# Kernel optimization log

Hardware: AMD Instinct MI355X
Metric: run time of the kernel (lower is better)

## Reference

```python
import jax, jax.numpy as jnp
import numpy as np

L, B, N_IN, N_OUT, BIDIR, K = 2048, 16, 256, 256, 2, 6


def setup_inputs() -> dict:
    key = jax.random.key(0)
    k1, k2 = jax.random.split(key, 2)
    x = jax.random.normal(k1, (L, B, N_IN), jnp.float32)
    val = (6.0 / (N_IN + N_OUT)) ** 0.5
    weight_in = jax.random.uniform(k2, (N_IN, BIDIR * N_OUT * K), jnp.float32, -val, val)
    bias_in = jnp.zeros((K * BIDIR * N_OUT,), jnp.float32)
    c1_init = jnp.zeros((B, BIDIR * N_OUT), jnp.float32)
    c2_init = jnp.zeros((B, BIDIR * N_OUT), jnp.float32)
    d_init = jnp.zeros((B, BIDIR * N_OUT), jnp.float32)
    return {"x": x, "weight_in": weight_in, "bias_in": bias_in,
            "c1_init": c1_init, "c2_init": c2_init, "d_init": d_init}


def _flip_dir1(a):
    # reverse time for the backward direction (dir index 1)
    return a.at[:, :, 1].set(jnp.flip(a[:, :, 1], axis=0))


def _sopa_forward(x, weight_in, bias_in, c1_init, c2_init, d_init):
    length, batch = x.shape[0], x.shape[1]
    # u_: [L, B, bidir, n_out, k]
    u = (x.reshape(-1, N_IN) @ weight_in).reshape(length, batch, BIDIR, N_OUT, K)
    bias = bias_in.reshape(K, BIDIR, N_OUT)  # [k, bidir, n_out]
    x1, x2, x3 = u[..., 0], u[..., 1], u[..., 2]
    f1 = jax.nn.sigmoid(u[..., 3] + bias[3])
    f2 = jax.nn.sigmoid(u[..., 4] + bias[4])
    # selfloop gate sigmoid(u[...,5]+bias[5]) is computed in the original but
    # unused by the recurrence, so it is omitted here (no effect on outputs).

    # flip time for direction 1 so one scan handles both directions
    x1f, x2f, x3f, f1f, f2f = (_flip_dir1(a) for a in (x1, x2, x3, f1, f2))

    c1_0 = c1_init.reshape(batch, BIDIR, N_OUT)
    c2_0 = c2_init.reshape(batch, BIDIR, N_OUT)
    d_0 = d_init.reshape(batch, BIDIR, N_OUT)

    def step(carry, inp):
        c1, c2, d = carry
        x1t, x2t, x3t, f1t, f2t = inp
        c1n = (c1 - x1t) * f1t + x1t
        tmp = x3t * d
        c2n = (c2 - tmp) * f2t + tmp
        return (c1n, c2n, x2t), (c1n, c2n)

    (c1_f, c2_f, d_f), (c1s, c2s) = jax.lax.scan(
        step, (c1_0, c2_0, d_0), (x1f, x2f, x3f, f1f, f2f))

    c1s = _flip_dir1(c1s)
    c2s = _flip_dir1(c2s)
    return (c1s, c2s,
            c1_f.reshape(batch, -1), c2_f.reshape(batch, -1), d_f.reshape(batch, -1))


def reference(x, weight_in, bias_in, c1_init, c2_init, d_init):
    return _sopa_forward(x, weight_in, bias_in, c1_init, c2_init, d_init)
```

## Files before the change

kernel.cpp:

```cpp
#include <hip/hip_runtime.h>
#include <cstdint>
#include <cstddef>

typedef unsigned short u16;
typedef unsigned int u32;
typedef __bf16 bf16x8 __attribute__((ext_vector_type(8)));
typedef float f32x4 __attribute__((ext_vector_type(4)));

#define SL 2048
#define NCH 8192
#define SEGS 64
#define SEGLEN 32

#define OFF_C2S 16777216
#define OFF_C1F 33554432
#define OFF_C2F 33562624
#define OFF_DF  33570816

__device__ __forceinline__ float bf2f(u16 u) {
  union { u32 i; float f; } v; v.i = ((u32)u) << 16; return v.f;
}
__device__ __forceinline__ u16 f2bf(float f) {
  union { float f; u32 i; } v; v.f = f;
  u32 x = v.i;
  return (u16)((x + 0x7fffu + ((x >> 16) & 1u)) >> 16);
}

__global__ __launch_bounds__(256) void repack_kernel(
    const float* __restrict__ W, u16* __restrict__ Wt) {
  int idx = blockIdx.x * 256 + threadIdx.x;
  int kk = idx & 255;
  int rest = idx >> 8;
  int ch2 = rest & 511;
  int p = rest >> 9;
  Wt[idx] = f2bf(W[(size_t)kk * 3072 + (ch2 >> 8) * 1536 + (ch2 & 255) * 6 + p]);
}

__global__ __launch_bounds__(256) void gemm_kernel(
    const float* __restrict__ x, const u16* __restrict__ Wt,
    const float* __restrict__ bias, u16* __restrict__ buf,
    u16* __restrict__ X2B, int t0c, int CHT) {
  __shared__ __align__(16) u16 As[2048 * 8];
  __shared__ __align__(16) u16 Bs[1024 * 8];
  const int tid = threadIdx.x;
  const int lane = tid & 63;
  const int wave = tid >> 6;
  const int wr = wave >> 1, wc = wave & 1;
  const int l15 = lane & 15, l4 = lane >> 4;
  const int rt = blockIdx.x;
  const int ch0 = blockIdx.y * 128;
  const int dir = ch0 >> 8;

#pragma unroll
  for (int i = 0; i < 8; ++i) {
    int chunk = tid + i * 256;
    int kb = chunk >> 6, m = chunk & 63;
    int tf = t0c + rt * 4 + (m >> 4);
    int ot = dir ? (SL - 1 - tf) : tf;
    int row = ot * 16 + (m & 15);
    const float* src = x + (size_t)row * 256 + kb * 8;
    f32x4 a = *(const f32x4*)src;
    f32x4 b = *(const f32x4*)(src + 4);
    union { bf16x8 v; u16 s[8]; } h;
#pragma unroll
    for (int j = 0; j < 4; ++j) { h.s[j] = f2bf(a[j]); h.s[4 + j] = f2bf(b[j]); }
    *(bf16x8*)(As + (size_t)chunk * 8) = h.v;
  }

  const size_t pstride = (size_t)CHT * NCH;
  for (int p = 0; p < 5; ++p) {
    f32x4 acc[2][4];
#pragma unroll
    for (int i = 0; i < 2; ++i)
#pragma unroll
      for (int j = 0; j < 4; ++j) acc[i][j] = (f32x4){0.f, 0.f, 0.f, 0.f};

    for (int kt = 0; kt < 4; ++kt) {
      bf16x8 rg[4];
#pragma unroll
      for (int i = 0; i < 4; ++i) {
        int chunk = tid + i * 256;
        int kbl = chunk >> 7, c = chunk & 127;
        rg[i] = *(const bf16x8*)(
            Wt + ((size_t)(p * 512 + ch0 + c) * 256 + kt * 64 + kbl * 8));
      }
      __syncthreads();
#pragma unroll
      for (int i = 0; i < 4; ++i) {
        int chunk = tid + i * 256;
        *(bf16x8*)(Bs + (size_t)chunk * 8) = rg[i];
      }
      __syncthreads();
#pragma unroll
      for (int h = 0; h < 2; ++h) {
        bf16x8 af[2], bfr[4];
#pragma unroll
        for (int i = 0; i < 2; ++i) {
          int kb = kt * 8 + h * 4 + l4;
          int m = wr * 32 + i * 16 + l15;
          af[i] = *(const bf16x8*)(As + (size_t)(kb * 64 + m) * 8);
        }
#pragma unroll
        for (int j = 0; j < 4; ++j) {
          int kbl = h * 4 + l4;
          int c = wc * 64 + j * 16 + l15;
          bfr[j] = *(const bf16x8*)(Bs + (size_t)(kbl * 128 + c) * 8);
        }
#pragma unroll
        for (int i = 0; i < 2; ++i)
#pragma unroll
          for (int j = 0; j < 4; ++j)
            acc[i][j] = __builtin_amdgcn_mfma_f32_16x16x32_bf16(
                af[i], bfr[j], acc[i][j], 0, 0, 0);
      }
    }

    u16* pl = buf + (size_t)p * pstride;
#pragma unroll
    for (int j = 0; j < 4; ++j) {
      int ch2 = ch0 + wc * 64 + j * 16 + l15;
      float bv = (p >= 3) ? bias[p * 512 + ch2] : 0.f;
#pragma unroll
      for (int i = 0; i < 2; ++i) {
#pragma unroll
        for (int r = 0; r < 4; ++r) {
          int row = wr * 32 + i * 16 + l4 * 4 + r;
          int tl = rt * 4 + (row >> 4);
          int b = row & 15;
          float v = acc[i][j][r];
          if (p >= 3) v = 1.f / (1.f + __expf(-(v + bv)));
          u16 hv = f2bf(v);
          int ch = b * 512 + ch2;
          pl[(size_t)tl * NCH + ch] = hv;
          if (p == 1) {
            int tf = t0c + tl;
            if ((tf & 31) == 31) X2B[(size_t)(tf >> 5) * NCH + ch] = hv;
          }
        }
      }
    }
  }
}

__global__ __launch_bounds__(256) void scanA_kernel(
    const u16* __restrict__ buf, const float* __restrict__ d_init,
    const u16* __restrict__ X2B,
    float* __restrict__ A1, float* __restrict__ B1,
    float* __restrict__ A2, float* __restrict__ B2, int c, int CHT) {
  int bid = blockIdx.x;
  int sl = bid >> 5, chg = bid & 31;
  int ch = chg * 256 + threadIdx.x;
  int s = c * (CHT / 32) + sl;
  size_t pstride = (size_t)CHT * NCH;
  const u16* p0 = buf;
  const u16* p1 = buf + pstride;
  const u16* p2 = buf + 2 * pstride;
  const u16* p3 = buf + 3 * pstride;
  const u16* p4 = buf + 4 * pstride;
  float x2prev = (s == 0) ? d_init[ch]
                          : bf2f(X2B[(size_t)(s - 1) * NCH + ch]);
  float a1 = 1.f, b1 = 0.f, a2 = 1.f, b2 = 0.f;
  size_t idx = (size_t)(sl * 32) * NCH + ch;
#pragma unroll 4
  for (int tt = 0; tt < SEGLEN; ++tt, idx += NCH) {
    float x1 = bf2f(p0[idx]), x2 = bf2f(p1[idx]), x3 = bf2f(p2[idx]);
    float f1 = bf2f(p3[idx]), f2 = bf2f(p4[idx]);
    a1 *= f1; b1 = f1 * b1 + (1.f - f1) * x1;
    float tmp = x3 * x2prev;
    a2 *= f2; b2 = f2 * b2 + (1.f - f2) * tmp;
    x2prev = x2;
  }
  int o = s * NCH + ch;
  A1[o] = a1; B1[o] = b1; A2[o] = a2; B2[o] = b2;
}

__global__ __launch_bounds__(256) void scanB_kernel(
    const float* __restrict__ A1, const float* __restrict__ B1,
    const float* __restrict__ A2, const float* __restrict__ B2,
    const float* __restrict__ c1_init, const float* __restrict__ c2_init,
    const u16* __restrict__ X2B,
    float* __restrict__ C1c, float* __restrict__ C2c, float* __restrict__ out) {
  int ch = blockIdx.x * 256 + threadIdx.x;
  float c1 = c1_init[ch], c2 = c2_init[ch];
#pragma unroll 8
  for (int s = 0; s < SEGS; ++s) {
    int o = s * NCH + ch;
    C1c[o] = c1; C2c[o] = c2;
    c1 = A1[o] * c1 + B1[o];
    c2 = A2[o] * c2 + B2[o];
  }
  out[OFF_C1F + ch] = c1;
  out[OFF_C2F + ch] = c2;
  out[OFF_DF + ch] = bf2f(X2B[(size_t)63 * NCH + ch]);
}

__global__ __launch_bounds__(256) void scanC_kernel(
    const u16* __restrict__ buf, const float* __restrict__ d_init,
    const u16* __restrict__ X2B,
    const float* __restrict__ C1c, const float* __restrict__ C2c,
    float* __restrict__ out, int c, int CHT) {
  int bid = blockIdx.x;
  int sl = bid >> 5, chg = bid & 31;
  int ch = chg * 256 + threadIdx.x;
  int s = c * (CHT / 32) + sl;
  size_t pstride = (size_t)CHT * NCH;
  const u16* p0 = buf;
  const u16* p1 = buf + pstride;
  const u16* p2 = buf + 2 * pstride;
  const u16* p3 = buf + 3 * pstride;
  const u16* p4 = buf + 4 * pstride;
  float x2prev = (s == 0) ? d_init[ch]
                          : bf2f(X2B[(size_t)(s - 1) * NCH + ch]);
  float c1 = C1c[s * NCH + ch];
  float c2 = C2c[s * NCH + ch];
  int dir = (ch >> 8) & 1;
  size_t idx = (size_t)(sl * 32) * NCH + ch;
#pragma unroll 4
  for (int tt = 0; tt < SEGLEN; ++tt, idx += NCH) {
    float x1 = bf2f(p0[idx]), x2 = bf2f(p1[idx]), x3 = bf2f(p2[idx]);
    float f1 = bf2f(p3[idx]), f2 = bf2f(p4[idx]);
    c1 = f1 * c1 + (1.f - f1) * x1;
    float tmp = x3 * x2prev;
    c2 = f2 * c2 + (1.f - f2) * tmp;
    x2prev = x2;
    int tfl = s * 32 + tt;
    int t_out = dir ? (SL - 1 - tfl) : tfl;
    size_t oidx = (size_t)t_out * NCH + ch;
    out[oidx] = c1;
    out[OFF_C2S + oidx] = c2;
  }
}

extern "C" void kernel_launch(void* const* d_in, const int* in_sizes, int n_in,
                              void* d_out, int out_size, void* d_ws, size_t ws_size,
                              hipStream_t stream) {
  const float* x    = (const float*)d_in[0];
  const float* W    = (const float*)d_in[1];
  const float* bias = (const float*)d_in[2];
  const float* c1i  = (const float*)d_in[3];
  const float* c2i  = (const float*)d_in[4];
  const float* di   = (const float*)d_in[5];
  float* out = (float*)d_out;

  uint8_t* w8 = (uint8_t*)d_ws;
  u16* Wt  = (u16*)w8;
  u16* X2B = (u16*)(w8 + 1310720ull);
  float* A1  = (float*)(w8 + 2359296ull);
  float* B1  = A1 + SEGS * NCH;
  float* A2  = B1 + SEGS * NCH;
  float* B2  = A2 + SEGS * NCH;
  float* C1c = B2 + SEGS * NCH;
  float* C2c = C1c + SEGS * NCH;
  const size_t FIXED = 2359296ull + 6ull * 2097152ull;
  u16* buf = (u16*)(w8 + FIXED);

  int NCHUNK = 64;
  size_t avail = (ws_size > FIXED) ? (ws_size - FIXED) : 0;
  for (int nc = 1; nc <= 64; nc <<= 1) {
    size_t need = (size_t)5 * (SL / nc) * NCH * 2;
    if (need <= avail) { NCHUNK = nc; break; }
  }
  const int CHT = SL / NCHUNK;

  hipLaunchKernelGGL(repack_kernel, dim3(2560), dim3(256), 0, stream, W, Wt);
  for (int c = 0; c < NCHUNK; ++c) {
    hipLaunchKernelGGL(gemm_kernel, dim3(CHT / 4, 4), dim3(256), 0, stream,
                       x, Wt, bias, buf, X2B, c * CHT, CHT);
    hipLaunchKernelGGL(scanA_kernel, dim3(CHT), dim3(256), 0, stream,
                       buf, di, X2B, A1, B1, A2, B2, c, CHT);
  }
  hipLaunchKernelGGL(scanB_kernel, dim3(32), dim3(256), 0, stream,
                     A1, B1, A2, B2, c1i, c2i, X2B, C1c, C2c, out);
  for (int c = 0; c < NCHUNK; ++c) {
    if (NCHUNK > 1)
      hipLaunchKernelGGL(gemm_kernel, dim3(CHT / 4, 4), dim3(256), 0, stream,
                         x, Wt, bias, buf, X2B, c * CHT, CHT);
    hipLaunchKernelGGL(scanC_kernel, dim3(CHT), dim3(256), 0, stream,
                       buf, di, X2B, C1c, C2c, out, c, CHT);
  }
}
```

Measured before the change: 373.8 us.

## Vectorize scans to 8 channels per thread, load GEMM B fragments directly

The scan kernels now handle 8 consecutive channels per thread with 16-byte bf16 loads and float4 stores, which cuts the block count and the number of memory instructions. The GEMM drops the LDS staging of weights and its two barriers per k-tile, loading B fragments straight from global memory. Float to bf16 conversion now uses the packed v_cvt_pk_bf16_f32 instruction, and an added barrier fixes a missing sync after the A tile is written to shared memory. In exchange, scan parallelism drops to 128 channel-threads per segment group, which lowers occupancy, and the direct global B loads depend on cache hits.

```diff
diff --git a/kernel.cpp b/kernel.cpp
--- a/kernel.cpp
+++ b/kernel.cpp
@@ -24,6 +24,11 @@
   union { float f; u32 i; } v; v.f = f;
   u32 x = v.i;
   return (u16)((x + 0x7fffu + ((x >> 16) & 1u)) >> 16);
+}
+__device__ __forceinline__ u32 cvtpk(float lo, float hi) {
+  u32 r;
+  asm("v_cvt_pk_bf16_f32 %0, %1, %2" : "=v"(r) : "v"(lo), "v"(hi));
+  return r;
 }
 
 __global__ __launch_bounds__(256) void repack_kernel(
@@ -41,7 +46,6 @@
     const float* __restrict__ bias, u16* __restrict__ buf,
     u16* __restrict__ X2B, int t0c, int CHT) {
   __shared__ __align__(16) u16 As[2048 * 8];
-  __shared__ __align__(16) u16 Bs[1024 * 8];
   const int tid = threadIdx.x;
   const int lane = tid & 63;
   const int wave = tid >> 6;
@@ -61,11 +65,14 @@
     const float* src = x + (size_t)row * 256 + kb * 8;
     f32x4 a = *(const f32x4*)src;
     f32x4 b = *(const f32x4*)(src + 4);
-    union { bf16x8 v; u16 s[8]; } h;
-#pragma unroll
-    for (int j = 0; j < 4; ++j) { h.s[j] = f2bf(a[j]); h.s[4 + j] = f2bf(b[j]); }
+    union { bf16x8 v; u32 u[4]; } h;
+    h.u[0] = cvtpk(a[0], a[1]);
+    h.u[1] = cvtpk(a[2], a[3]);
+    h.u[2] = cvtpk(b[0], b[1]);
+    h.u[3] = cvtpk(b[2], b[3]);
     *(bf16x8*)(As + (size_t)chunk * 8) = h.v;
   }
+  __syncthreads();
 
   const size_t pstride = (size_t)CHT * NCH;
   for (int p = 0; p < 5; ++p) {
@@ -75,37 +82,22 @@
 #pragma unroll
       for (int j = 0; j < 4; ++j) acc[i][j] = (f32x4){0.f, 0.f, 0.f, 0.f};
 
+    const u16* Wp = Wt + (size_t)(p * 512 + ch0 + wc * 64 + l15) * 256;
+
+#pragma unroll
     for (int kt = 0; kt < 4; ++kt) {
-      bf16x8 rg[4];
-#pragma unroll
-      for (int i = 0; i < 4; ++i) {
-        int chunk = tid + i * 256;
-        int kbl = chunk >> 7, c = chunk & 127;
-        rg[i] = *(const bf16x8*)(
-            Wt + ((size_t)(p * 512 + ch0 + c) * 256 + kt * 64 + kbl * 8));
-      }
-      __syncthreads();
-#pragma unroll
-      for (int i = 0; i < 4; ++i) {
-        int chunk = tid + i * 256;
-        *(bf16x8*)(Bs + (size_t)chunk * 8) = rg[i];
-      }
-      __syncthreads();
 #pragma unroll
       for (int h = 0; h < 2; ++h) {
-        bf16x8 af[2], bfr[4];
-#pragma unroll
-        for (int i = 0; i < 2; ++i) {
-          int kb = kt * 8 + h * 4 + l4;
-          int m = wr * 32 + i * 16 + l15;
-          af[i] = *(const bf16x8*)(As + (size_t)(kb * 64 + m) * 8);
-        }
-#pragma unroll
-        for (int j = 0; j < 4; ++j) {
-          int kbl = h * 4 + l4;
-          int c = wc * 64 + j * 16 + l15;
-          bfr[j] = *(const bf16x8*)(Bs + (size_t)(kbl * 128 + c) * 8);
-        }
+        const int kb = kt * 8 + h * 4 + l4;
+        bf16x8 bfr[4];
+#pragma unroll
+        for (int j = 0; j < 4; ++j)
+          bfr[j] = *(const bf16x8*)(Wp + (size_t)j * 16 * 256 + kb * 8);
+        bf16x8 af[2];
+#pragma unroll
+        for (int i = 0; i < 2; ++i)
+          af[i] = *(const bf16x8*)(
+              As + (size_t)(kb * 64 + wr * 32 + i * 16 + l15) * 8);
 #pragma unroll
         for (int i = 0; i < 2; ++i)
 #pragma unroll
@@ -122,19 +114,26 @@
       float bv = (p >= 3) ? bias[p * 512 + ch2] : 0.f;
 #pragma unroll
       for (int i = 0; i < 2; ++i) {
-#pragma unroll
-        for (int r = 0; r < 4; ++r) {
-          int row = wr * 32 + i * 16 + l4 * 4 + r;
-          int tl = rt * 4 + (row >> 4);
-          int b = row & 15;
-          float v = acc[i][j][r];
-          if (p >= 3) v = 1.f / (1.f + __expf(-(v + bv)));
-          u16 hv = f2bf(v);
+        int tl = rt * 4 + wr * 2 + i;
+        int tf = t0c + tl;
+        bool rec = (p == 1) && ((tf & 31) == 31);
+#pragma unroll
+        for (int r = 0; r < 4; r += 2) {
+          float va = acc[i][j][r], vb = acc[i][j][r + 1];
+          if (p >= 3) {
+            va = 1.f / (1.f + __expf(-(va + bv)));
+            vb = 1.f / (1.f + __expf(-(vb + bv)));
+          }
+          u32 pk = cvtpk(va, vb);
+          int b = l4 * 4 + r;
           int ch = b * 512 + ch2;
-          pl[(size_t)tl * NCH + ch] = hv;
-          if (p == 1) {
-            int tf = t0c + tl;
-            if ((tf & 31) == 31) X2B[(size_t)(tf >> 5) * NCH + ch] = hv;
+          size_t o = (size_t)tl * NCH + ch;
+          pl[o] = (u16)pk;
+          pl[o + 512] = (u16)(pk >> 16);
+          if (rec) {
+            size_t xo = (size_t)(tf >> 5) * NCH + ch;
+            X2B[xo] = (u16)pk;
+            X2B[xo + 512] = (u16)(pk >> 16);
           }
         }
       }
@@ -148,30 +147,57 @@
     float* __restrict__ A1, float* __restrict__ B1,
     float* __restrict__ A2, float* __restrict__ B2, int c, int CHT) {
   int bid = blockIdx.x;
-  int sl = bid >> 5, chg = bid & 31;
-  int ch = chg * 256 + threadIdx.x;
+  int sl = bid >> 2, chb = bid & 3;
+  int ch = chb * 2048 + threadIdx.x * 8;
   int s = c * (CHT / 32) + sl;
   size_t pstride = (size_t)CHT * NCH;
-  const u16* p0 = buf;
-  const u16* p1 = buf + pstride;
-  const u16* p2 = buf + 2 * pstride;
-  const u16* p3 = buf + 3 * pstride;
-  const u16* p4 = buf + 4 * pstride;
-  float x2prev = (s == 0) ? d_init[ch]
-                          : bf2f(X2B[(size_t)(s - 1) * NCH + ch]);
-  float a1 = 1.f, b1 = 0.f, a2 = 1.f, b2 = 0.f;
-  size_t idx = (size_t)(sl * 32) * NCH + ch;
+  const u16* p0 = buf + (size_t)(sl * 32) * NCH + ch;
+
+  float x2p[8];
+  if (s == 0) {
+    f32x4 d0 = *(const f32x4*)(d_init + ch);
+    f32x4 d1 = *(const f32x4*)(d_init + ch + 4);
+#pragma unroll
+    for (int r = 0; r < 4; ++r) { x2p[r] = d0[r]; x2p[4 + r] = d1[r]; }
+  } else {
+    union { bf16x8 v; u16 s[8]; } xv;
+    xv.v = *(const bf16x8*)(X2B + (size_t)(s - 1) * NCH + ch);
+#pragma unroll
+    for (int r = 0; r < 8; ++r) x2p[r] = bf2f(xv.s[r]);
+  }
+
+  float a1[8], b1[8], a2[8], b2[8];
+#pragma unroll
+  for (int r = 0; r < 8; ++r) { a1[r] = 1.f; b1[r] = 0.f; a2[r] = 1.f; b2[r] = 0.f; }
+
 #pragma unroll 4
-  for (int tt = 0; tt < SEGLEN; ++tt, idx += NCH) {
-    float x1 = bf2f(p0[idx]), x2 = bf2f(p1[idx]), x3 = bf2f(p2[idx]);
-    float f1 = bf2f(p3[idx]), f2 = bf2f(p4[idx]);
-    a1 *= f1; b1 = f1 * b1 + (1.f - f1) * x1;
-    float tmp = x3 * x2prev;
-    a2 *= f2; b2 = f2 * b2 + (1.f - f2) * tmp;
-    x2prev = x2;
-  }
-  int o = s * NCH + ch;
-  A1[o] = a1; B1[o] = b1; A2[o] = a2; B2[o] = b2;
+  for (int tt = 0; tt < SEGLEN; ++tt) {
+    size_t off = (size_t)tt * NCH;
+    union U { bf16x8 v; u16 s[8]; } v0, v1, v2, v3, v4;
+    v0.v = *(const bf16x8*)(p0 + off);
+    v1.v = *(const bf16x8*)(p0 + pstride + off);
+    v2.v = *(const bf16x8*)(p0 + 2 * pstride + off);
+    v3.v = *(const bf16x8*)(p0 + 3 * pstride + off);
+    v4.v = *(const bf16x8*)(p0 + 4 * pstride + off);
+#pragma unroll
+    for (int r = 0; r < 8; ++r) {
+      float x1 = bf2f(v0.s[r]), x2 = bf2f(v1.s[r]), x3 = bf2f(v2.s[r]);
+      float f1 = bf2f(v3.s[r]), f2 = bf2f(v4.s[r]);
+      a1[r] *= f1; b1[r] = f1 * b1[r] + (1.f - f1) * x1;
+      float tmp = x3 * x2p[r];
+      a2[r] *= f2; b2[r] = f2 * b2[r] + (1.f - f2) * tmp;
+      x2p[r] = x2;
+    }
+  }
+  size_t o = (size_t)s * NCH + ch;
+  *(f32x4*)(A1 + o) = (f32x4){a1[0], a1[1], a1[2], a1[3]};
+  *(f32x4*)(A1 + o + 4) = (f32x4){a1[4], a1[5], a1[6], a1[7]};
+  *(f32x4*)(B1 + o) = (f32x4){b1[0], b1[1], b1[2], b1[3]};
+  *(f32x4*)(B1 + o + 4) = (f32x4){b1[4], b1[5], b1[6], b1[7]};
+  *(f32x4*)(A2 + o) = (f32x4){a2[0], a2[1], a2[2], a2[3]};
+  *(f32x4*)(A2 + o + 4) = (f32x4){a2[4], a2[5], a2[6], a2[7]};
+  *(f32x4*)(B2 + o) = (f32x4){b2[0], b2[1], b2[2], b2[3]};
+  *(f32x4*)(B2 + o + 4) = (f32x4){b2[4], b2[5], b2[6], b2[7]};
 }
 
 __global__ __launch_bounds__(256) void scanB_kernel(
@@ -200,34 +226,66 @@
     const float* __restrict__ C1c, const float* __restrict__ C2c,
     float* __restrict__ out, int c, int CHT) {
   int bid = blockIdx.x;
-  int sl = bid >> 5, chg = bid & 31;
-  int ch = chg * 256 + threadIdx.x;
+  int sl = bid >> 2, chb = bid & 3;
+  int ch = chb * 2048 + threadIdx.x * 8;
   int s = c * (CHT / 32) + sl;
   size_t pstride = (size_t)CHT * NCH;
-  const u16* p0 = buf;
-  const u16* p1 = buf + pstride;
-  const u16* p2 = buf + 2 * pstride;
-  const u16* p3 = buf + 3 * pstride;
-  const u16* p4 = buf + 4 * pstride;
-  float x2prev = (s == 0) ? d_init[ch]
-                          : bf2f(X2B[(size_t)(s - 1) * NCH + ch]);
-  float c1 = C1c[s * NCH + ch];
-  float c2 = C2c[s * NCH + ch];
+  const u16* p0 = buf + (size_t)(sl * 32) * NCH + ch;
   int dir = (ch >> 8) & 1;
-  size_t idx = (size_t)(sl * 32) * NCH + ch;
-#pragma unroll 4
-  for (int tt = 0; tt < SEGLEN; ++tt, idx += NCH) {
-    float x1 = bf2f(p0[idx]), x2 = bf2f(p1[idx]), x3 = bf2f(p2[idx]);
-    float f1 = bf2f(p3[idx]), f2 = bf2f(p4[idx]);
-    c1 = f1 * c1 + (1.f - f1) * x1;
-    float tmp = x3 * x2prev;
-    c2 = f2 * c2 + (1.f - f2) * tmp;
-    x2prev = x2;
+
+  float x2p[8];
+  if (s == 0) {
+    f32x4 d0 = *(const f32x4*)(d_init + ch);
+    f32x4 d1 = *(const f32x4*)(d_init + ch + 4);
+#pragma unroll
+    for (int r = 0; r < 4; ++r) { x2p[r] = d0[r]; x2p[4 + r] = d1[r]; }
+  } else {
+    union { bf16x8 v; u16 s[8]; } xv;
+    xv.v = *(const bf16x8*)(X2B + (size_t)(s - 1) * NCH + ch);
+#pragma unroll
+    for (int r = 0; r < 8; ++r) x2p[r] = bf2f(xv.s[r]);
+  }
+
+  float c1[8], c2[8];
+  {
+    size_t o = (size_t)s * NCH + ch;
+    f32x4 u0 = *(const f32x4*)(C1c + o);
+    f32x4 u1 = *(const f32x4*)(C1c + o + 4);
+    f32x4 w0 = *(const f32x4*)(C2c + o);
+    f32x4 w1 = *(const f32x4*)(C2c + o + 4);
+#pragma unroll
+    for (int r = 0; r < 4; ++r) {
+      c1[r] = u0[r]; c1[4 + r] = u1[r];
+      c2[r] = w0[r]; c2[4 + r] = w1[r];
+    }
+  }
+
+#pragma unroll 2
+  for (int tt = 0; tt < SEGLEN; ++tt) {
+    size_t off = (size_t)tt * NCH;
+    union U { bf16x8 v; u16 s[8]; } v0, v1, v2, v3, v4;
+    v0.v = *(const bf16x8*)(p0 + off);
+    v1.v = *(const bf16x8*)(p0 + pstride + off);
+    v2.v = *(const bf16x8*)(p0 + 2 * pstride + off);
+    v3.v = *(const bf16x8*)(p0 + 3 * pstride + off);
+    v4.v = *(const bf16x8*)(p0 + 4 * pstride + off);
+#pragma unroll
+    for (int r = 0; r < 8; ++r) {
+      float x1 = bf2f(v0.s[r]), x2 = bf2f(v1.s[r]), x3 = bf2f(v2.s[r]);
+      float f1 = bf2f(v3.s[r]), f2 = bf2f(v4.s[r]);
+      c1[r] = f1 * c1[r] + (1.f - f1) * x1;
+      float tmp = x3 * x2p[r];
+      c2[r] = f2 * c2[r] + (1.f - f2) * tmp;
+      x2p[r] = x2;
+    }
     int tfl = s * 32 + tt;
     int t_out = dir ? (SL - 1 - tfl) : tfl;
-    size_t oidx = (size_t)t_out * NCH + ch;
-    out[oidx] = c1;
-    out[OFF_C2S + oidx] = c2;
+    float* o1 = out + (size_t)t_out * NCH + ch;
+    *(f32x4*)o1       = (f32x4){c1[0], c1[1], c1[2], c1[3]};
+    *(f32x4*)(o1 + 4) = (f32x4){c1[4], c1[5], c1[6], c1[7]};
+    float* o2 = o1 + OFF_C2S;
+    *(f32x4*)o2       = (f32x4){c2[0], c2[1], c2[2], c2[3]};
+    *(f32x4*)(o2 + 4) = (f32x4){c2[4], c2[5], c2[6], c2[7]};
   }
 }
 
@@ -266,7 +324,7 @@
   for (int c = 0; c < NCHUNK; ++c) {
     hipLaunchKernelGGL(gemm_kernel, dim3(CHT / 4, 4), dim3(256), 0, stream,
                        x, Wt, bias, buf, X2B, c * CHT, CHT);
-    hipLaunchKernelGGL(scanA_kernel, dim3(CHT), dim3(256), 0, stream,
+    hipLaunchKernelGGL(scanA_kernel, dim3((CHT / 32) * 4), dim3(256), 0, stream,
                        buf, di, X2B, A1, B1, A2, B2, c, CHT);
   }
   hipLaunchKernelGGL(scanB_kernel, dim3(32), dim3(256), 0, stream,
@@ -275,7 +333,7 @@
     if (NCHUNK > 1)
       hipLaunchKernelGGL(gemm_kernel, dim3(CHT / 4, 4), dim3(256), 0, stream,
                          x, Wt, bias, buf, X2B, c * CHT, CHT);
-    hipLaunchKernelGGL(scanC_kernel, dim3(CHT), dim3(256), 0, stream,
+    hipLaunchKernelGGL(scanC_kernel, dim3((CHT / 32) * 4), dim3(256), 0, stream,
                        buf, di, X2B, C1c, C2c, out, c, CHT);
   }
 }
```

Measured after the change: 443.0 us. 1.19x slower.

## Fuse projection GEMM into segment scans, recompute GEMM instead of buffering activations

Applied to the files above, without the earlier changes.

Replaces the chunked GEMM-then-scan pipeline with two fused kernels that compute the projection with MFMA in registers and immediately run the segment scan, recomputing the GEMM in the final pass instead of storing bf16 activations. x is pre-converted to a bf16 layout and weights are repacked into MFMA fragment order so B fragments load directly from global memory without LDS. The d-carry dependence across segments is folded into a G2 coefficient so segment summaries no longer need the previous segment's x2, and outputs use nontemporal stores. This removes the large intermediate buffer traffic and many kernel launches, at the cost of doing the GEMM twice and reading fragments uncached through global memory.

```diff
diff --git a/kernel.cpp b/kernel.cpp
--- a/kernel.cpp
+++ b/kernel.cpp
@@ -10,224 +10,272 @@
 #define SL 2048
 #define NCH 8192
 #define SEGS 64
-#define SEGLEN 32
 
 #define OFF_C2S 16777216
 #define OFF_C1F 33554432
 #define OFF_C2F 33562624
 #define OFF_DF  33570816
 
-__device__ __forceinline__ float bf2f(u16 u) {
-  union { u32 i; float f; } v; v.i = ((u32)u) << 16; return v.f;
-}
 __device__ __forceinline__ u16 f2bf(float f) {
   union { float f; u32 i; } v; v.f = f;
   u32 x = v.i;
   return (u16)((x + 0x7fffu + ((x >> 16) & 1u)) >> 16);
 }
+__device__ __forceinline__ u32 cvtpk(float lo, float hi) {
+  u32 r;
+  asm("v_cvt_pk_bf16_f32 %0, %1, %2" : "=v"(r) : "v"(lo), "v"(hi));
+  return r;
+}
+__device__ __forceinline__ float sigmoidf(float v) {
+  return 1.f / (1.f + __expf(-v));
+}
+
+__global__ __launch_bounds__(256) void xconv_kernel(
+    const float* __restrict__ x, u16* __restrict__ xb) {
+  int t8 = blockIdx.x * 256 + threadIdx.x;
+  int kb = t8 & 31;
+  int b  = (t8 >> 5) & 15;
+  int ot = t8 >> 9;
+  const float* src = x + (((size_t)(ot * 16 + b)) << 8) + kb * 8;
+  f32x4 a = *(const f32x4*)src;
+  f32x4 c = *(const f32x4*)(src + 4);
+  union { bf16x8 v; u32 u[4]; } h;
+  h.u[0] = cvtpk(a[0], a[1]);
+  h.u[1] = cvtpk(a[2], a[3]);
+  h.u[2] = cvtpk(c[0], c[1]);
+  h.u[3] = cvtpk(c[2], c[3]);
+  *(bf16x8*)(xb + ((size_t)ot << 12) + kb * 128 + b * 8) = h.v;
+}
 
 __global__ __launch_bounds__(256) void repack_kernel(
     const float* __restrict__ W, u16* __restrict__ Wt) {
   int idx = blockIdx.x * 256 + threadIdx.x;
-  int kk = idx & 255;
-  int rest = idx >> 8;
-  int ch2 = rest & 511;
-  int p = rest >> 9;
+  int kk8 = idx & 7;
+  int lane = (idx >> 3) & 63;
+  int h  = (idx >> 9) & 1;
+  int kt = (idx >> 10) & 3;
+  int cg = (idx >> 12) & 31;
+  int p  = idx >> 17;
+  int ch2 = cg * 16 + (lane & 15);
+  int kk  = (kt * 8 + h * 4 + (lane >> 4)) * 8 + kk8;
   Wt[idx] = f2bf(W[(size_t)kk * 3072 + (ch2 >> 8) * 1536 + (ch2 & 255) * 6 + p]);
 }
 
-__global__ __launch_bounds__(256) void gemm_kernel(
-    const float* __restrict__ x, const u16* __restrict__ Wt,
-    const float* __restrict__ bias, u16* __restrict__ buf,
-    u16* __restrict__ X2B, int t0c, int CHT) {
-  __shared__ __align__(16) u16 As[2048 * 8];
-  __shared__ __align__(16) u16 Bs[1024 * 8];
+__global__ __launch_bounds__(256, 2) void fusedA_kernel(
+    const u16* __restrict__ xb, const u16* __restrict__ Wt,
+    const float* __restrict__ bias,
+    float* __restrict__ A1, float* __restrict__ B1,
+    float* __restrict__ A2, float* __restrict__ B2k,
+    float* __restrict__ G2, float* __restrict__ X2B) {
   const int tid = threadIdx.x;
   const int lane = tid & 63;
-  const int wave = tid >> 6;
-  const int wr = wave >> 1, wc = wave & 1;
+  const int wc = tid >> 6;
   const int l15 = lane & 15, l4 = lane >> 4;
-  const int rt = blockIdx.x;
-  const int ch0 = blockIdx.y * 128;
-  const int dir = ch0 >> 8;
-
-#pragma unroll
-  for (int i = 0; i < 8; ++i) {
-    int chunk = tid + i * 256;
-    int kb = chunk >> 6, m = chunk & 63;
-    int tf = t0c + rt * 4 + (m >> 4);
-    int ot = dir ? (SL - 1 - tf) : tf;
-    int row = ot * 16 + (m & 15);
-    const float* src = x + (size_t)row * 256 + kb * 8;
-    f32x4 a = *(const f32x4*)src;
-    f32x4 b = *(const f32x4*)(src + 4);
-    union { bf16x8 v; u16 s[8]; } h;
-#pragma unroll
-    for (int j = 0; j < 4; ++j) { h.s[j] = f2bf(a[j]); h.s[4 + j] = f2bf(b[j]); }
-    *(bf16x8*)(As + (size_t)chunk * 8) = h.v;
-  }
-
-  const size_t pstride = (size_t)CHT * NCH;
-  for (int p = 0; p < 5; ++p) {
-    f32x4 acc[2][4];
-#pragma unroll
-    for (int i = 0; i < 2; ++i)
-#pragma unroll
-      for (int j = 0; j < 4; ++j) acc[i][j] = (f32x4){0.f, 0.f, 0.f, 0.f};
-
+  const int s = blockIdx.x;
+  const int bc = blockIdx.y;
+  const int dir = bc >> 2;
+  const int ch2 = bc * 64 + wc * 16 + l15;
+  const int fb0 = (bc * 4 + wc) * 8;
+
+  const float bv3 = bias[1536 + ch2];
+  const float bv4 = bias[2048 + ch2];
+
+  float a1[4], b1[4], a2[4], b2[4], g2[4], x2p[4];
+#pragma unroll
+  for (int r = 0; r < 4; ++r) {
+    a1[r] = 1.f; b1[r] = 0.f; a2[r] = 1.f; b2[r] = 0.f;
+    g2[r] = 0.f; x2p[r] = 0.f;
+  }
+
+  for (int rt = 0; rt < 8; ++rt) {
+    const u16* ab0; const u16* ab1; const u16* ab2; const u16* ab3;
+    {
+      int tf = s * 32 + rt * 4;
+      int o0 = dir ? (SL - 1 - tf) : tf;
+      int o1 = dir ? (o0 - 1) : (o0 + 1);
+      int o2 = dir ? (o0 - 2) : (o0 + 2);
+      int o3 = dir ? (o0 - 3) : (o0 + 3);
+      size_t lo = (size_t)(l4 * 128 + l15 * 8);
+      ab0 = xb + ((size_t)o0 << 12) + lo;
+      ab1 = xb + ((size_t)o1 << 12) + lo;
+      ab2 = xb + ((size_t)o2 << 12) + lo;
+      ab3 = xb + ((size_t)o3 << 12) + lo;
+    }
+
+    f32x4 acc[5][4];
+#pragma unroll
+    for (int p = 0; p < 5; ++p)
+#pragma unroll
+      for (int i = 0; i < 4; ++i) acc[p][i] = (f32x4){0.f, 0.f, 0.f, 0.f};
+
+#pragma unroll
     for (int kt = 0; kt < 4; ++kt) {
-      bf16x8 rg[4];
-#pragma unroll
-      for (int i = 0; i < 4; ++i) {
-        int chunk = tid + i * 256;
-        int kbl = chunk >> 7, c = chunk & 127;
-        rg[i] = *(const bf16x8*)(
-            Wt + ((size_t)(p * 512 + ch0 + c) * 256 + kt * 64 + kbl * 8));
-      }
-      __syncthreads();
-#pragma unroll
-      for (int i = 0; i < 4; ++i) {
-        int chunk = tid + i * 256;
-        *(bf16x8*)(Bs + (size_t)chunk * 8) = rg[i];
-      }
-      __syncthreads();
 #pragma unroll
       for (int h = 0; h < 2; ++h) {
-        bf16x8 af[2], bfr[4];
-#pragma unroll
-        for (int i = 0; i < 2; ++i) {
-          int kb = kt * 8 + h * 4 + l4;
-          int m = wr * 32 + i * 16 + l15;
-          af[i] = *(const bf16x8*)(As + (size_t)(kb * 64 + m) * 8);
-        }
-#pragma unroll
-        for (int j = 0; j < 4; ++j) {
-          int kbl = h * 4 + l4;
-          int c = wc * 64 + j * 16 + l15;
-          bfr[j] = *(const bf16x8*)(Bs + (size_t)(kbl * 128 + c) * 8);
-        }
-#pragma unroll
-        for (int i = 0; i < 2; ++i)
-#pragma unroll
-          for (int j = 0; j < 4; ++j)
-            acc[i][j] = __builtin_amdgcn_mfma_f32_16x16x32_bf16(
-                af[i], bfr[j], acc[i][j], 0, 0, 0);
-      }
-    }
-
-    u16* pl = buf + (size_t)p * pstride;
-#pragma unroll
-    for (int j = 0; j < 4; ++j) {
-      int ch2 = ch0 + wc * 64 + j * 16 + l15;
-      float bv = (p >= 3) ? bias[p * 512 + ch2] : 0.f;
-#pragma unroll
-      for (int i = 0; i < 2; ++i) {
-#pragma unroll
-        for (int r = 0; r < 4; ++r) {
-          int row = wr * 32 + i * 16 + l4 * 4 + r;
-          int tl = rt * 4 + (row >> 4);
-          int b = row & 15;
-          float v = acc[i][j][r];
-          if (p >= 3) v = 1.f / (1.f + __expf(-(v + bv)));
-          u16 hv = f2bf(v);
-          int ch = b * 512 + ch2;
-          pl[(size_t)tl * NCH + ch] = hv;
-          if (p == 1) {
-            int tf = t0c + tl;
-            if ((tf & 31) == 31) X2B[(size_t)(tf >> 5) * NCH + ch] = hv;
-          }
+        const int kb4 = (kt * 8 + h * 4) * 128;
+        bf16x8 af[4];
+        af[0] = *(const bf16x8*)(ab0 + kb4);
+        af[1] = *(const bf16x8*)(ab1 + kb4);
+        af[2] = *(const bf16x8*)(ab2 + kb4);
+        af[3] = *(const bf16x8*)(ab3 + kb4);
+        const int fb = fb0 + kt * 2 + h;
+#pragma unroll
+        for (int p = 0; p < 5; ++p) {
+          bf16x8 bfr = *(const bf16x8*)(
+              Wt + (size_t)(p * 256 + fb) * 512 + lane * 8);
+#pragma unroll
+          for (int i = 0; i < 4; ++i)
+            acc[p][i] = __builtin_amdgcn_mfma_f32_16x16x32_bf16(
+                af[i], bfr, acc[p][i], 0, 0, 0);
         }
       }
     }
-  }
-}
-
-__global__ __launch_bounds__(256) void scanA_kernel(
-    const u16* __restrict__ buf, const float* __restrict__ d_init,
-    const u16* __restrict__ X2B,
-    float* __restrict__ A1, float* __restrict__ B1,
-    float* __restrict__ A2, float* __restrict__ B2, int c, int CHT) {
-  int bid = blockIdx.x;
-  int sl = bid >> 5, chg = bid & 31;
-  int ch = chg * 256 + threadIdx.x;
-  int s = c * (CHT / 32) + sl;
-  size_t pstride = (size_t)CHT * NCH;
-  const u16* p0 = buf;
-  const u16* p1 = buf + pstride;
-  const u16* p2 = buf + 2 * pstride;
-  const u16* p3 = buf + 3 * pstride;
-  const u16* p4 = buf + 4 * pstride;
-  float x2prev = (s == 0) ? d_init[ch]
-                          : bf2f(X2B[(size_t)(s - 1) * NCH + ch]);
-  float a1 = 1.f, b1 = 0.f, a2 = 1.f, b2 = 0.f;
-  size_t idx = (size_t)(sl * 32) * NCH + ch;
-#pragma unroll 4
-  for (int tt = 0; tt < SEGLEN; ++tt, idx += NCH) {
-    float x1 = bf2f(p0[idx]), x2 = bf2f(p1[idx]), x3 = bf2f(p2[idx]);
-    float f1 = bf2f(p3[idx]), f2 = bf2f(p4[idx]);
-    a1 *= f1; b1 = f1 * b1 + (1.f - f1) * x1;
-    float tmp = x3 * x2prev;
-    a2 *= f2; b2 = f2 * b2 + (1.f - f2) * tmp;
-    x2prev = x2;
-  }
-  int o = s * NCH + ch;
-  A1[o] = a1; B1[o] = b1; A2[o] = a2; B2[o] = b2;
+
+    const bool first = (rt == 0);
+#pragma unroll
+    for (int i = 0; i < 4; ++i) {
+#pragma unroll
+      for (int r = 0; r < 4; ++r) {
+        float x1 = acc[0][i][r], x2v = acc[1][i][r], x3 = acc[2][i][r];
+        float f1 = sigmoidf(acc[3][i][r] + bv3);
+        float f2 = sigmoidf(acc[4][i][r] + bv4);
+        a1[r] *= f1;
+        b1[r] = f1 * b1[r] + (1.f - f1) * x1;
+        float tmp = x3 * x2p[r];
+        a2[r] *= f2;
+        b2[r] = f2 * b2[r] + (1.f - f2) * tmp;
+        g2[r] = (first && i == 0) ? (1.f - f2) * x3 : g2[r] * f2;
+        x2p[r] = x2v;
+      }
+    }
+  }
+
+  const int chb = (l4 * 4) * 512 + ch2;
+  const size_t o = (size_t)s * NCH + chb;
+#pragma unroll
+  for (int r = 0; r < 4; ++r) {
+    size_t oo = o + (size_t)r * 512;
+    A1[oo] = a1[r]; B1[oo] = b1[r]; A2[oo] = a2[r];
+    B2k[oo] = b2[r]; G2[oo] = g2[r]; X2B[oo] = x2p[r];
+  }
 }
 
 __global__ __launch_bounds__(256) void scanB_kernel(
     const float* __restrict__ A1, const float* __restrict__ B1,
-    const float* __restrict__ A2, const float* __restrict__ B2,
+    const float* __restrict__ A2, const float* __restrict__ B2k,
+    const float* __restrict__ G2, const float* __restrict__ X2B,
     const float* __restrict__ c1_init, const float* __restrict__ c2_init,
-    const u16* __restrict__ X2B,
-    float* __restrict__ C1c, float* __restrict__ C2c, float* __restrict__ out) {
+    const float* __restrict__ d_init,
+    float* __restrict__ C1c, float* __restrict__ C2c,
+    float* __restrict__ out) {
   int ch = blockIdx.x * 256 + threadIdx.x;
-  float c1 = c1_init[ch], c2 = c2_init[ch];
+  float c1 = c1_init[ch], c2 = c2_init[ch], d0 = d_init[ch];
 #pragma unroll 8
   for (int s = 0; s < SEGS; ++s) {
     int o = s * NCH + ch;
     C1c[o] = c1; C2c[o] = c2;
     c1 = A1[o] * c1 + B1[o];
-    c2 = A2[o] * c2 + B2[o];
+    c2 = A2[o] * c2 + (B2k[o] + G2[o] * d0);
+    d0 = X2B[o];
   }
   out[OFF_C1F + ch] = c1;
   out[OFF_C2F + ch] = c2;
-  out[OFF_DF + ch] = bf2f(X2B[(size_t)63 * NCH + ch]);
-}
-
-__global__ __launch_bounds__(256) void scanC_kernel(
-    const u16* __restrict__ buf, const float* __restrict__ d_init,
-    const u16* __restrict__ X2B,
+  out[OFF_DF + ch] = d0;
+}
+
+__global__ __launch_bounds__(256, 2) void fusedC_kernel(
+    const u16* __restrict__ xb, const u16* __restrict__ Wt,
+    const float* __restrict__ bias, const float* __restrict__ d_init,
+    const float* __restrict__ X2B,
     const float* __restrict__ C1c, const float* __restrict__ C2c,
-    float* __restrict__ out, int c, int CHT) {
-  int bid = blockIdx.x;
-  int sl = bid >> 5, chg = bid & 31;
-  int ch = chg * 256 + threadIdx.x;
-  int s = c * (CHT / 32) + sl;
-  size_t pstride = (size_t)CHT * NCH;
-  const u16* p0 = buf;
-  const u16* p1 = buf + pstride;
-  const u16* p2 = buf + 2 * pstride;
-  const u16* p3 = buf + 3 * pstride;
-  const u16* p4 = buf + 4 * pstride;
-  float x2prev = (s == 0) ? d_init[ch]
-                          : bf2f(X2B[(size_t)(s - 1) * NCH + ch]);
-  float c1 = C1c[s * NCH + ch];
-  float c2 = C2c[s * NCH + ch];
-  int dir = (ch >> 8) & 1;
-  size_t idx = (size_t)(sl * 32) * NCH + ch;
-#pragma unroll 4
-  for (int tt = 0; tt < SEGLEN; ++tt, idx += NCH) {
-    float x1 = bf2f(p0[idx]), x2 = bf2f(p1[idx]), x3 = bf2f(p2[idx]);
-    float f1 = bf2f(p3[idx]), f2 = bf2f(p4[idx]);
-    c1 = f1 * c1 + (1.f - f1) * x1;
-    float tmp = x3 * x2prev;
-    c2 = f2 * c2 + (1.f - f2) * tmp;
-    x2prev = x2;
-    int tfl = s * 32 + tt;
-    int t_out = dir ? (SL - 1 - tfl) : tfl;
-    size_t oidx = (size_t)t_out * NCH + ch;
-    out[oidx] = c1;
-    out[OFF_C2S + oidx] = c2;
+    float* __restrict__ out) {
+  const int tid = threadIdx.x;
+  const int lane = tid & 63;
+  const int wc = tid >> 6;
+  const int l15 = lane & 15, l4 = lane >> 4;
+  const int s = blockIdx.x;
+  const int bc = blockIdx.y;
+  const int dir = bc >> 2;
+  const int ch2 = bc * 64 + wc * 16 + l15;
+  const int fb0 = (bc * 4 + wc) * 8;
+
+  const float bv3 = bias[1536 + ch2];
+  const float bv4 = bias[2048 + ch2];
+
+  const int chb = (l4 * 4) * 512 + ch2;
+  float c1[4], c2[4], x2p[4];
+  {
+    size_t o = (size_t)s * NCH + chb;
+#pragma unroll
+    for (int r = 0; r < 4; ++r) {
+      c1[r] = C1c[o + r * 512];
+      c2[r] = C2c[o + r * 512];
+      x2p[r] = (s == 0) ? d_init[chb + r * 512] : X2B[o - NCH + r * 512];
+    }
+  }
+
+  for (int rt = 0; rt < 8; ++rt) {
+    const u16* ab0; const u16* ab1; const u16* ab2; const u16* ab3;
+    {
+      int tf = s * 32 + rt * 4;
+      int o0 = dir ? (SL - 1 - tf) : tf;
+      int o1 = dir ? (o0 - 1) : (o0 + 1);
+      int o2 = dir ? (o0 - 2) : (o0 + 2);
+      int o3 = dir ? (o0 - 3) : (o0 + 3);
+      size_t lo = (size_t)(l4 * 128 + l15 * 8);
+      ab0 = xb + ((size_t)o0 << 12) + lo;
+      ab1 = xb + ((size_t)o1 << 12) + lo;
+      ab2 = xb + ((size_t)o2 << 12) + lo;
+      ab3 = xb + ((size_t)o3 << 12) + lo;
+    }
+
+    f32x4 acc[5][4];
+#pragma unroll
+    for (int p = 0; p < 5; ++p)
+#pragma unroll
+      for (int i = 0; i < 4; ++i) acc[p][i] = (f32x4){0.f, 0.f, 0.f, 0.f};
+
+#pragma unroll
+    for (int kt = 0; kt < 4; ++kt) {
+#pragma unroll
+      for (int h = 0; h < 2; ++h) {
+        const int kb4 = (kt * 8 + h * 4) * 128;
+        bf16x8 af[4];
+        af[0] = *(const bf16x8*)(ab0 + kb4);
+        af[1] = *(const bf16x8*)(ab1 + kb4);
+        af[2] = *(const bf16x8*)(ab2 + kb4);
+        af[3] = *(const bf16x8*)(ab3 + kb4);
+        const int fb = fb0 + kt * 2 + h;
+#pragma unroll
+        for (int p = 0; p < 5; ++p) {
+          bf16x8 bfr = *(const bf16x8*)(
+              Wt + (size_t)(p * 256 + fb) * 512 + lane * 8);
+#pragma unroll
+          for (int i = 0; i < 4; ++i)
+            acc[p][i] = __builtin_amdgcn_mfma_f32_16x16x32_bf16(
+                af[i], bfr, acc[p][i], 0, 0, 0);
+        }
+      }
+    }
+
+#pragma unroll
+    for (int i = 0; i < 4; ++i) {
+      int tfl = s * 32 + rt * 4 + i;
+      int t_out = dir ? (SL - 1 - tfl) : tfl;
+      float* orow = out + (size_t)t_out * NCH + chb;
+#pragma unroll
+      for (int r = 0; r < 4; ++r) {
+        float x1 = acc[0][i][r], x2v = acc[1][i][r], x3 = acc[2][i][r];
+        float f1 = sigmoidf(acc[3][i][r] + bv3);
+        float f2 = sigmoidf(acc[4][i][r] + bv4);
+        c1[r] = f1 * c1[r] + (1.f - f1) * x1;
+        float tmp = x3 * x2p[r];
+        c2[r] = f2 * c2[r] + (1.f - f2) * tmp;
+        x2p[r] = x2v;
+        __builtin_nontemporal_store(c1[r], orow + r * 512);
+        __builtin_nontemporal_store(c2[r], orow + OFF_C2S + (size_t)r * 512);
+      }
+    }
   }
 }
 
@@ -244,38 +292,22 @@
 
   uint8_t* w8 = (uint8_t*)d_ws;
   u16* Wt  = (u16*)w8;
-  u16* X2B = (u16*)(w8 + 1310720ull);
-  float* A1  = (float*)(w8 + 2359296ull);
-  float* B1  = A1 + SEGS * NCH;
-  float* A2  = B1 + SEGS * NCH;
-  float* B2  = A2 + SEGS * NCH;
-  float* C1c = B2 + SEGS * NCH;
+  u16* xb  = (u16*)(w8 + 1310720ull);
+  float* X2B = (float*)(w8 + 18087936ull);
+  float* A1  = (float*)(w8 + 20185088ull);
+  float* B1  = A1  + SEGS * NCH;
+  float* A2  = B1  + SEGS * NCH;
+  float* B2k = A2  + SEGS * NCH;
+  float* G2  = B2k + SEGS * NCH;
+  float* C1c = G2  + SEGS * NCH;
   float* C2c = C1c + SEGS * NCH;
-  const size_t FIXED = 2359296ull + 6ull * 2097152ull;
-  u16* buf = (u16*)(w8 + FIXED);
-
-  int NCHUNK = 64;
-  size_t avail = (ws_size > FIXED) ? (ws_size - FIXED) : 0;
-  for (int nc = 1; nc <= 64; nc <<= 1) {
-    size_t need = (size_t)5 * (SL / nc) * NCH * 2;
-    if (need <= avail) { NCHUNK = nc; break; }
-  }
-  const int CHT = SL / NCHUNK;
-
+
+  hipLaunchKernelGGL(xconv_kernel, dim3(4096), dim3(256), 0, stream, x, xb);
   hipLaunchKernelGGL(repack_kernel, dim3(2560), dim3(256), 0, stream, W, Wt);
-  for (int c = 0; c < NCHUNK; ++c) {
-    hipLaunchKernelGGL(gemm_kernel, dim3(CHT / 4, 4), dim3(256), 0, stream,
-                       x, Wt, bias, buf, X2B, c * CHT, CHT);
-    hipLaunchKernelGGL(scanA_kernel, dim3(CHT), dim3(256), 0, stream,
-                       buf, di, X2B, A1, B1, A2, B2, c, CHT);
-  }
+  hipLaunchKernelGGL(fusedA_kernel, dim3(64, 8), dim3(256), 0, stream,
+                     xb, Wt, bias, A1, B1, A2, B2k, G2, X2B);
   hipLaunchKernelGGL(scanB_kernel, dim3(32), dim3(256), 0, stream,
-                     A1, B1, A2, B2, c1i, c2i, X2B, C1c, C2c, out);
-  for (int c = 0; c < NCHUNK; ++c) {
-    if (NCHUNK > 1)
-      hipLaunchKernelGGL(gemm_kernel, dim3(CHT / 4, 4), dim3(256), 0, stream,
-                         x, Wt, bias, buf, X2B, c * CHT, CHT);
-    hipLaunchKernelGGL(scanC_kernel, dim3(CHT), dim3(256), 0, stream,
-                       buf, di, X2B, C1c, C2c, out, c, CHT);
-  }
-}
+                     A1, B1, A2, B2k, G2, X2B, c1i, c2i, di, C1c, C2c, out);
+  hipLaunchKernelGGL(fusedC_kernel, dim3(64, 8), dim3(256), 0, stream,
+                     xb, Wt, bias, di, X2B, C1c, C2c, out);
+}
```

New measurement: 370.3 us. No clear change (-1.0%).
